# Kernel optimization log

Hardware: AMD Instinct MI355X
Metric: run time of the kernel (lower is better)

The kernel has to match this reference:

```python
import jax, jax.numpy as jnp
import numpy as np

BIAS = 1.0
SIGMA = 0.5
EPS = 1e-5


def _mrf_loss(gen, tar):
    # gen, tar: [N, C, H, W]
    N, C, H, W = tar.shape
    meanT = jnp.mean(tar, axis=1, keepdims=True)
    g = gen - meanT
    t = tar - meanT
    g = g / jnp.linalg.norm(g, ord=2, axis=1, keepdims=True)
    t = t / jnp.linalg.norm(t, ord=2, axis=1, keepdims=True)
    # 1x1-patch conv2d with target patches as filters == per-pixel cosine
    # correlation matrix: [N, P=H*W (target positions), H, W (gen positions)]
    tp = t.reshape(N, C, H * W)
    cd = jnp.einsum('nchw,ncp->nphw', g, tp)
    cd = -(cd - 1.0) / 2.0  # cosine distance in [0, 1]
    div = jnp.min(cd, axis=1, keepdims=True)
    rel = cd / (div + EPS)
    e = jnp.exp((BIAS - rel) / SIGMA)
    cs = e / jnp.sum(e, axis=1, keepdims=True)  # sum-normalize over P
    k_max_nc = jnp.max(cs.reshape(N, H * W, -1), axis=2)  # max over gen HW
    div_mrf = jnp.mean(k_max_nc, axis=1)
    return jnp.sum(-jnp.log(div_mrf))


def setup_inputs() -> dict:
    key = jax.random.key(0)
    k1, k2, k3, k4 = jax.random.split(key, 4)
    return {
        'gen3': jax.random.normal(k1, (4, 256, 56, 56), dtype=jnp.float32),
        'tar3': jax.random.normal(k2, (4, 256, 56, 56), dtype=jnp.float32),
        'gen4': jax.random.normal(k3, (4, 512, 28, 28), dtype=jnp.float32),
        'tar4': jax.random.normal(k4, (4, 512, 28, 28), dtype=jnp.float32),
    }


def reference(gen3, tar3, gen4, tar4):
    # weights = [0, 0, 0.5, 1, 0] over VGG relu1..relu5 features
    return 0.5 * _mrf_loss(gen3, tar3) + 1.0 * _mrf_loss(gen4, tar4)
```

## Files before the change

### kernel.cpp

```cpp
#include <hip/hip_runtime.h>
#include <math.h>

typedef __bf16 bf16x8 __attribute__((ext_vector_type(8)));
typedef float f32x4 __attribute__((ext_vector_type(4)));

#define EPSV 1e-5f
#define GLB(p) ((__attribute__((address_space(1))) void*)(p))
#define LDS(p) ((__attribute__((address_space(3))) void*)(p))

__device__ __forceinline__ unsigned fkey(float f) {
  unsigned b = __float_as_uint(f);
  return (b & 0x80000000u) ? ~b : (b | 0x80000000u);
}
__device__ __forceinline__ float funkey(unsigned k) {
  return __uint_as_float((k & 0x80000000u) ? (k & 0x7fffffffu) : ~k);
}

__global__ __launch_bounds__(256) void norm_kernel(
    const float* __restrict__ g3, const float* __restrict__ t3,
    __bf16* __restrict__ G3, __bf16* __restrict__ T3,
    const float* __restrict__ g4, const float* __restrict__ t4,
    __bf16* __restrict__ G4, __bf16* __restrict__ T4,
    float* __restrict__ ksum)
{
  if (blockIdx.z == 0 && blockIdx.y == 0 && threadIdx.x < 8)
    ksum[threadIdx.x] = 0.f;
  int lay = blockIdx.z >> 2, n = blockIdx.z & 3;
  const float *gen, *tar; __bf16 *Gh, *Th; int C, P, Ppad, PT, NWORK, NTOT, NG;
  if (lay == 0) { gen = g3; tar = t3; Gh = G3; Th = T3; C = 256; P = 3136; Ppad = 3200; PT = 32; NWORK = 98; NTOT = 100; NG = 8; }
  else          { gen = g4; tar = t4; Gh = G4; Th = T4; C = 512; P = 784;  Ppad = 896;  PT = 16; NWORK = 49; NTOT = 56;  NG = 16; }
  if (blockIdx.y >= (unsigned)NTOT) return;
  int pl, cg;
  if (lay == 0) { pl = threadIdx.x & 31; cg = threadIdx.x >> 5; }
  else          { pl = threadIdx.x & 15; cg = threadIdx.x >> 4; }
  int c0 = cg * 32;

  if (blockIdx.y >= (unsigned)NWORK) {
    int p = P + (blockIdx.y - NWORK) * PT + pl;
    if (p < Ppad) {
      __bf16* tp = Th + ((size_t)n * Ppad + p) * C + c0;
      __bf16* gp = Gh + ((size_t)n * Ppad + p) * C + c0;
      bf16x8 z;
      for (int j = 0; j < 8; j++) z[j] = (__bf16)0.f;
      for (int j = 0; j < 32; j += 8) { *(bf16x8*)(tp + j) = z; *(bf16x8*)(gp + j) = z; }
    }
    return;
  }

  int p = blockIdx.y * PT + pl;
  const float* tb = tar + (size_t)n * C * P + (size_t)c0 * P + p;
  const float* gb = gen + (size_t)n * C * P + (size_t)c0 * P + p;
  float tv[32], gv[32];
  float st = 0.f, sst = 0.f, sg = 0.f, ssg = 0.f;
#pragma unroll
  for (int j = 0; j < 32; j++) {
    tv[j] = tb[(size_t)j * P];
    gv[j] = gb[(size_t)j * P];
  }
#pragma unroll
  for (int j = 0; j < 32; j++) {
    st += tv[j]; sst += tv[j] * tv[j];
    sg += gv[j]; ssg += gv[j] * gv[j];
  }
  __shared__ f32x4 red[16][32];
  red[cg][pl] = f32x4{st, sst, sg, ssg};
  __syncthreads();
  for (int h = NG >> 1; h > 0; h >>= 1) {
    if (cg < h) {
      f32x4 a = red[cg][pl], b = red[cg + h][pl];
      red[cg][pl] = f32x4{a[0] + b[0], a[1] + b[1], a[2] + b[2], a[3] + b[3]};
    }
    __syncthreads();
  }
  f32x4 s = red[0][pl];
  float m = s[0] / (float)C;
  float vt = s[1] - s[0] * s[0] / (float)C;
  float vg = s[3] - 2.f * m * s[2] + (float)C * m * m;
  float it = rsqrtf(fmaxf(vt, 1e-30f));
  float ig = rsqrtf(fmaxf(vg, 1e-30f));
  __bf16* tp = Th + ((size_t)n * Ppad + p) * C + c0;
  __bf16* gp = Gh + ((size_t)n * Ppad + p) * C + c0;
#pragma unroll
  for (int j0 = 0; j0 < 32; j0 += 8) {
    bf16x8 to, go;
    for (int j = 0; j < 8; j++) {
      to[j] = (__bf16)((tv[j0 + j] - m) * it);
      go[j] = (__bf16)((gv[j0 + j] - m) * ig);
    }
    *(bf16x8*)(tp + j0) = to;
    *(bf16x8*)(gp + j0) = go;
  }
}

__global__ __launch_bounds__(256, 3) void gemm_kernel(
    const __bf16* __restrict__ A3, const __bf16* __restrict__ B3,
    __bf16* __restrict__ So3, unsigned* __restrict__ dk3,
    const __bf16* __restrict__ A4, const __bf16* __restrict__ B4,
    __bf16* __restrict__ So4, unsigned* __restrict__ dk4)
{
  __shared__ __attribute__((aligned(16))) char smem[37888];

  int id = blockIdx.x;
  const __bf16 *A, *B; __bf16* S; unsigned* dk;
  int C, Ppad, Qpad, Preal, NT, n, t;
  if (id < 2500) {
    n = id / 625; t = id - n * 625;
    A = A3; B = B3; S = So3; dk = dk3; C = 256; Ppad = 3200; Qpad = 3200; Preal = 3136; NT = 25;
  } else {
    id -= 2500;
    n = id / 49; t = id - n * 49;
    A = A4; B = B4; S = So4; dk = dk4; C = 512; Ppad = 896;  Qpad = 896;  Preal = 784;  NT = 7;
  }
  int bpb = NT * 8;
  int b = t / bpb, r = t - b * bpb;
  int rem = NT - b * 8;
  int h = rem < 8 ? rem : 8;
  int pt = b * 8 + r % h, qt = r / h;
  int p0 = pt * 128, q0 = qt * 128;

  int tid = threadIdx.x;
  int w = tid >> 6, lane = tid & 63;
  int lm = lane & 15, lq = lane >> 4;
  int wrow = (w >> 1) * 64, wcol = (w & 1) * 64;

  int srow = tid >> 2;
  int scol = ((tid & 3) ^ ((tid >> 3) & 3)) * 8;
  const __bf16* gA = A + ((size_t)n * Ppad + p0 + srow) * C + scol;
  const __bf16* gB = B + ((size_t)n * Qpad + q0 + srow) * C + scol;
  size_t rowoff = (size_t)64 * C;

  int sl = lq ^ ((lm >> 1) & 3);
  int aoff = (wrow + lm) * 64 + sl * 16;
  int boff = (wcol + lm) * 64 + sl * 16;

  f32x4 acc[4][4];
  for (int i = 0; i < 4; i++)
    for (int j = 0; j < 4; j++)
      acc[i][j] = f32x4{0.f, 0.f, 0.f, 0.f};

  for (int k0 = 0; k0 < C; k0 += 64) {
    __syncthreads();
#pragma unroll
    for (int sub = 0; sub < 2; sub++) {
      int kk = k0 + sub * 32;
      char* a = smem + sub * 8192 + w * 1024;
      char* bb = smem + 16384 + sub * 8192 + w * 1024;
      __builtin_amdgcn_global_load_lds(GLB(gA + kk), LDS(a), 16, 0, 0);
      __builtin_amdgcn_global_load_lds(GLB(gA + rowoff + kk), LDS(a + 4096), 16, 0, 0);
      __builtin_amdgcn_global_load_lds(GLB(gB + kk), LDS(bb), 16, 0, 0);
      __builtin_amdgcn_global_load_lds(GLB(gB + rowoff + kk), LDS(bb + 4096), 16, 0, 0);
    }
    __syncthreads();
#pragma unroll
    for (int sub = 0; sub < 2; sub++) {
      const char* ab = smem + sub * 8192;
      const char* bb = smem + 16384 + sub * 8192;
      bf16x8 af[4], bf[4];
      for (int i = 0; i < 4; i++) af[i] = *(const bf16x8*)(ab + aoff + i * 1024);
      for (int j = 0; j < 4; j++) bf[j] = *(const bf16x8*)(bb + boff + j * 1024);
      for (int i = 0; i < 4; i++)
        for (int j = 0; j < 4; j++)
          acc[i][j] = __builtin_amdgcn_mfma_f32_16x16x32_bf16(af[i], bf[j], acc[i][j], 0, 0, 0);
    }
  }

  float cm[4] = {-INFINITY, -INFINITY, -INFINITY, -INFINITY};
  for (int i = 0; i < 4; i++)
    for (int j = 0; j < 4; j++)
      for (int ri = 0; ri < 4; ri++) {
        int pr = p0 + wrow + i * 16 + lq * 4 + ri;
        if (pr < Preal) cm[j] = fmaxf(cm[j], (float)(__bf16)acc[i][j][ri]);
      }

  __syncthreads();
  for (int i = 0; i < 4; i++) {
    for (int j = 0; j < 4; j++) {
      int row = wrow + i * 16 + lq * 4;
      int col = wcol + j * 16 + lm;
      for (int ri = 0; ri < 4; ri++)
        *(__bf16*)(smem + (row + ri) * 296 + col * 2) = (__bf16)acc[i][j][ri];
    }
  }
  __syncthreads();
  __bf16* Sb = S + (size_t)n * Ppad * Qpad;
  int rr = tid >> 4, cc8 = (tid & 15) * 8;
  for (int r8 = 0; r8 < 8; r8++) {
    int row = r8 * 16 + rr;
    bf16x8 v = *(const bf16x8*)(smem + row * 296 + cc8 * 2);
    __builtin_nontemporal_store(v, (bf16x8*)(Sb + (size_t)(p0 + row) * Qpad + q0 + cc8));
  }

  for (int j = 0; j < 4; j++) {
    float v = cm[j];
    v = fmaxf(v, __shfl_xor(v, 16, 64));
    v = fmaxf(v, __shfl_xor(v, 32, 64));
    if (lq == 0 && v > -INFINITY) {
      int qc = q0 + wcol + j * 16 + lm;
      atomicMax(&dk[(size_t)n * Qpad + qc], fkey(v));
    }
  }
}

__global__ __launch_bounds__(256) void z_kernel(
    const __bf16* __restrict__ S3, const unsigned* __restrict__ dk3, float* __restrict__ Zp3,
    const __bf16* __restrict__ S4, const unsigned* __restrict__ dk4, float* __restrict__ Zp4)
{
  int id = blockIdx.x;
  const __bf16* S; const unsigned* dk; float* Zp;
  int Ppad, Qreal, Qpad, NSL, SLAB, n, qx, sy;
  if (id < 784) {
    n = id / 196; int r = id - n * 196; sy = r >> 1; qx = r & 1;
    S = S3; dk = dk3; Zp = Zp3; Ppad = 3200; Qreal = 3136; Qpad = 3200; NSL = 98; SLAB = 32;
  } else {
    id -= 784;
    n = id / 49; sy = id - n * 49; qx = 0;
    S = S4; dk = dk4; Zp = Zp4; Ppad = 896;  Qreal = 784;  Qpad = 896;  NSL = 49; SLAB = 16;
  }
  int q = (qx * 256 + threadIdx.x) * 8;
  if (q >= Qreal) return;
  float idv[8], nid[8];
  const unsigned* dkp = dk + (size_t)n * Qpad + q;
#pragma unroll
  for (int j = 0; j < 8; j++) {
    float mx = funkey(dkp[j]);
    float d = 0.5f * (1.f - mx) + EPSV;
    idv[j] = 1.f / d;
    nid[j] = -idv[j];
  }
  int p0 = sy * SLAB;
  const __bf16* Sp = S + (size_t)n * Ppad * Qpad + q;
  float acc[8] = {0.f, 0.f, 0.f, 0.f, 0.f, 0.f, 0.f, 0.f};
  for (int pb = 0; pb < SLAB; pb += 8) {
    bf16x8 sv[8];
#pragma unroll
    for (int r = 0; r < 8; r++)
      sv[r] = *(const bf16x8*)(Sp + (size_t)(p0 + pb + r) * Qpad);
#pragma unroll
    for (int r = 0; r < 8; r++)
      for (int j = 0; j < 8; j++)
        acc[j] += __expf(fmaf((float)sv[r][j], idv[j], nid[j]));
  }
  float* zp = Zp + ((size_t)n * NSL + sy) * Qpad + q;
  *(f32x4*)zp = f32x4{acc[0], acc[1], acc[2], acc[3]};
  *(f32x4*)(zp + 4) = f32x4{acc[4], acc[5], acc[6], acc[7]};
}

__global__ __launch_bounds__(256) void reduce_kernel(
    const float* __restrict__ Zp3, const unsigned* __restrict__ dk3,
    float* __restrict__ invd3, float* __restrict__ c3,
    const float* __restrict__ Zp4, const unsigned* __restrict__ dk4,
    float* __restrict__ invd4, float* __restrict__ c4)
{
  int lay = blockIdx.y >> 2, n = blockIdx.y & 3;
  const float* Zp; const unsigned* dk; float *invd, *c; int Qreal, Qpad, NSL;
  if (lay == 0) { Zp = Zp3; dk = dk3; invd = invd3; c = c3; Qreal = 3136; Qpad = 3200; NSL = 98; }
  else          { Zp = Zp4; dk = dk4; invd = invd4; c = c4; Qreal = 784;  Qpad = 896;  NSL = 49; }
  int q = blockIdx.x * 256 + threadIdx.x;
  if (q >= Qreal) return;
  float s0 = 0.f, s1 = 0.f, s2 = 0.f, s3 = 0.f;
  int sl = 0;
  for (; sl + 4 <= NSL; sl += 4) {
    s0 += Zp[((size_t)n * NSL + sl) * Qpad + q];
    s1 += Zp[((size_t)n * NSL + sl + 1) * Qpad + q];
    s2 += Zp[((size_t)n * NSL + sl + 2) * Qpad + q];
    s3 += Zp[((size_t)n * NSL + sl + 3) * Qpad + q];
  }
  for (; sl < NSL; sl++) s0 += Zp[((size_t)n * NSL + sl) * Qpad + q];
  float s = (s0 + s1) + (s2 + s3);
  float mx = funkey(dk[(size_t)n * Qpad + q]);
  float d = 0.5f * (1.f - mx) + EPSV;
  float idv = 1.f / d;
  invd[(size_t)n * Qpad + q] = idv;
  c[(size_t)n * Qpad + q] = -logf(s) - idv;
}

template<int ROWS>
__device__ __forceinline__ float rowmax_partial(
    const __bf16* __restrict__ Sp, const float* __restrict__ idp,
    const float* __restrict__ cp, int nq8, int Qpad)
{
  float m[ROWS];
#pragma unroll
  for (int r = 0; r < ROWS; r++) m[r] = -INFINITY;
  for (int i = threadIdx.x; i < nq8; i += 256) {
    f32x4 i0 = *(const f32x4*)(idp + (size_t)i * 8);
    f32x4 i1 = *(const f32x4*)(idp + (size_t)i * 8 + 4);
    f32x4 c0 = *(const f32x4*)(cp + (size_t)i * 8);
    f32x4 c1 = *(const f32x4*)(cp + (size_t)i * 8 + 4);
#pragma unroll
    for (int r = 0; r < ROWS; r++) {
      bf16x8 sv = *(const bf16x8*)(Sp + (size_t)r * Qpad + (size_t)i * 8);
#pragma unroll
      for (int j = 0; j < 4; j++)
        m[r] = fmaxf(m[r], fmaf((float)sv[j], i0[j], c0[j]));
#pragma unroll
      for (int j = 0; j < 4; j++)
        m[r] = fmaxf(m[r], fmaf((float)sv[j + 4], i1[j], c1[j]));
    }
  }
#pragma unroll
  for (int r = 0; r < ROWS; r++)
    for (int off = 32; off > 0; off >>= 1)
      m[r] = fmaxf(m[r], __shfl_xor(m[r], off, 64));
  __shared__ float red[4][ROWS];
  int w = threadIdx.x >> 6;
  if ((threadIdx.x & 63) == 0)
#pragma unroll
    for (int r = 0; r < ROWS; r++) red[w][r] = m[r];
  __syncthreads();
  float e = 0.f;
  if (threadIdx.x < ROWS) {
    int r = threadIdx.x;
    float mr = fmaxf(fmaxf(red[0][r], red[1][r]), fmaxf(red[2][r], red[3][r]));
    e = __expf(mr);
  }
  if (threadIdx.x < 64) {
#pragma unroll
    for (int off = 1; off < ROWS; off <<= 1)
      e += __shfl_xor(e, off, 64);
  }
  return e;
}

__global__ __launch_bounds__(256) void rowmax_kernel(
    const __bf16* __restrict__ S3, const float* __restrict__ invd3,
    const float* __restrict__ c3,
    const __bf16* __restrict__ S4, const float* __restrict__ invd4,
    const float* __restrict__ c4, float* __restrict__ ksum)
{
  int id = blockIdx.x;
  if (id < 392) {
    int n = id / 98, blk = id - n * 98;
    const __bf16* Sp = S3 + ((size_t)n * 3200 + blk * 32) * 3200;
    float e = rowmax_partial<32>(Sp, invd3 + (size_t)n * 3200,
                                 c3 + (size_t)n * 3200, 392, 3200);
    if (threadIdx.x == 0) atomicAdd(&ksum[n], e);
  } else {
    id -= 392;
    int n = id / 49, blk = id - n * 49;
    const __bf16* Sp = S4 + ((size_t)n * 896 + blk * 16) * 896;
    float e = rowmax_partial<16>(Sp, invd4 + (size_t)n * 896,
                                 c4 + (size_t)n * 896, 98, 896);
    if (threadIdx.x == 0) atomicAdd(&ksum[4 + n], e);
  }
}

__global__ void final_kernel(const float* __restrict__ ksum, float* __restrict__ out)
{
  if (threadIdx.x == 0) {
    float lp3 = logf(3136.f), lp4 = logf(784.f);
    float total = 0.f;
    for (int n = 0; n < 4; n++) total += 0.5f * (lp3 - logf(ksum[n]));
    for (int n = 0; n < 4; n++) total += 1.0f * (lp4 - logf(ksum[4 + n]));
    out[0] = total;
  }
}

extern "C" void kernel_launch(void* const* d_in, const int* in_sizes, int n_in,
                              void* d_out, int out_size, void* d_ws, size_t ws_size,
                              hipStream_t stream)
{
  const float* gen3 = (const float*)d_in[0];
  const float* tar3 = (const float*)d_in[1];
  const float* gen4 = (const float*)d_in[2];
  const float* tar4 = (const float*)d_in[3];

  char* ws = (char*)d_ws;
  size_t off = 0;
  auto take = [&](size_t bytes) { char* p = ws + off; off += bytes; return p; };

  unsigned* divkey3 = (unsigned*)take(51200);
  unsigned* divkey4 = (unsigned*)take(14336);
  size_t zero_bytes = off;
  __bf16* That3 = (__bf16*)take(6553600);
  __bf16* Ghat3 = (__bf16*)take(6553600);
  __bf16* That4 = (__bf16*)take(3670016);
  __bf16* Ghat4 = (__bf16*)take(3670016);
  __bf16* S3    = (__bf16*)take(81920000);
  __bf16* S4    = (__bf16*)take(6422528);
  float*  Zp3   = (float*) take(5017600);
  float*  Zp4   = (float*) take(702464);
  float* invd3  = (float*)take(51200);
  float* c3     = (float*)take(51200);
  float* ksum   = (float*)take(51200);
  float* invd4  = (float*)take(14336);
  float* c4     = (float*)take(14336);

  hipMemsetAsync(divkey3, 0, zero_bytes, stream);

  norm_kernel<<<dim3(1, 100, 8), 256, 0, stream>>>(gen3, tar3, Ghat3, That3,
                                                   gen4, tar4, Ghat4, That4, ksum);
  gemm_kernel<<<2696, 256, 0, stream>>>(That3, Ghat3, S3, divkey3,
                                        That4, Ghat4, S4, divkey4);
  z_kernel<<<980, 256, 0, stream>>>(S3, divkey3, Zp3,
                                    S4, divkey4, Zp4);
  reduce_kernel<<<dim3(13, 8), 256, 0, stream>>>(Zp3, divkey3, invd3, c3,
                                                 Zp4, divkey4, invd4, c4);
  rowmax_kernel<<<588, 256, 0, stream>>>(S3, invd3, c3,
                                         S4, invd4, c4, ksum);
  final_kernel<<<1, 64, 0, stream>>>(ksum, (float*)d_out);
}
```

Before: 195.3 us.

## Remap GEMM block ids across XCDs, use exp2 and atomic Z accumulation

```diff
diff --git a/kernel.cpp b/kernel.cpp
--- a/kernel.cpp
+++ b/kernel.cpp
@@ -100,7 +100,8 @@
 {
   __shared__ __attribute__((aligned(16))) char smem[37888];
 
-  int id = blockIdx.x;
+  int bid = blockIdx.x;
+  int id = (bid & 7) * 337 + (bid >> 3);
   const __bf16 *A, *B; __bf16* S; unsigned* dk;
   int C, Ppad, Qpad, Preal, NT, n, t;
   if (id < 2500) {
@@ -202,30 +203,31 @@
 }
 
 __global__ __launch_bounds__(256) void z_kernel(
-    const __bf16* __restrict__ S3, const unsigned* __restrict__ dk3, float* __restrict__ Zp3,
-    const __bf16* __restrict__ S4, const unsigned* __restrict__ dk4, float* __restrict__ Zp4)
+    const __bf16* __restrict__ S3, const unsigned* __restrict__ dk3, float* __restrict__ Z3,
+    const __bf16* __restrict__ S4, const unsigned* __restrict__ dk4, float* __restrict__ Z4)
 {
   int id = blockIdx.x;
-  const __bf16* S; const unsigned* dk; float* Zp;
-  int Ppad, Qreal, Qpad, NSL, SLAB, n, qx, sy;
+  const __bf16* S; const unsigned* dk; float* Z;
+  int Ppad, Qreal, Qpad, SLAB, n, qx, sy;
   if (id < 784) {
     n = id / 196; int r = id - n * 196; sy = r >> 1; qx = r & 1;
-    S = S3; dk = dk3; Zp = Zp3; Ppad = 3200; Qreal = 3136; Qpad = 3200; NSL = 98; SLAB = 32;
+    S = S3; dk = dk3; Z = Z3; Ppad = 3200; Qreal = 3136; Qpad = 3200; SLAB = 32;
   } else {
     id -= 784;
     n = id / 49; sy = id - n * 49; qx = 0;
-    S = S4; dk = dk4; Zp = Zp4; Ppad = 896;  Qreal = 784;  Qpad = 896;  NSL = 49; SLAB = 16;
+    S = S4; dk = dk4; Z = Z4; Ppad = 896;  Qreal = 784;  Qpad = 896;  SLAB = 16;
   }
   int q = (qx * 256 + threadIdx.x) * 8;
   if (q >= Qreal) return;
-  float idv[8], nid[8];
+  float idv2[8], nid2[8];
   const unsigned* dkp = dk + (size_t)n * Qpad + q;
 #pragma unroll
   for (int j = 0; j < 8; j++) {
     float mx = funkey(dkp[j]);
     float d = 0.5f * (1.f - mx) + EPSV;
-    idv[j] = 1.f / d;
-    nid[j] = -idv[j];
+    float iv = 1.4426950408889634f / d;
+    idv2[j] = iv;
+    nid2[j] = -iv;
   }
   int p0 = sy * SLAB;
   const __bf16* Sp = S + (size_t)n * Ppad * Qpad + q;
@@ -238,35 +240,26 @@
 #pragma unroll
     for (int r = 0; r < 8; r++)
       for (int j = 0; j < 8; j++)
-        acc[j] += __expf(fmaf((float)sv[r][j], idv[j], nid[j]));
-  }
-  float* zp = Zp + ((size_t)n * NSL + sy) * Qpad + q;
-  *(f32x4*)zp = f32x4{acc[0], acc[1], acc[2], acc[3]};
-  *(f32x4*)(zp + 4) = f32x4{acc[4], acc[5], acc[6], acc[7]};
+        acc[j] += exp2f(fmaf((float)sv[r][j], idv2[j], nid2[j]));
+  }
+  float* zp = Z + (size_t)n * Qpad + q;
+#pragma unroll
+  for (int j = 0; j < 8; j++) atomicAdd(zp + j, acc[j]);
 }
 
 __global__ __launch_bounds__(256) void reduce_kernel(
-    const float* __restrict__ Zp3, const unsigned* __restrict__ dk3,
+    const float* __restrict__ Z3, const unsigned* __restrict__ dk3,
     float* __restrict__ invd3, float* __restrict__ c3,
-    const float* __restrict__ Zp4, const unsigned* __restrict__ dk4,
+    const float* __restrict__ Z4, const unsigned* __restrict__ dk4,
     float* __restrict__ invd4, float* __restrict__ c4)
 {
   int lay = blockIdx.y >> 2, n = blockIdx.y & 3;
-  const float* Zp; const unsigned* dk; float *invd, *c; int Qreal, Qpad, NSL;
-  if (lay == 0) { Zp = Zp3; dk = dk3; invd = invd3; c = c3; Qreal = 3136; Qpad = 3200; NSL = 98; }
-  else          { Zp = Zp4; dk = dk4; invd = invd4; c = c4; Qreal = 784;  Qpad = 896;  NSL = 49; }
+  const float* Z; const unsigned* dk; float *invd, *c; int Qreal, Qpad;
+  if (lay == 0) { Z = Z3; dk = dk3; invd = invd3; c = c3; Qreal = 3136; Qpad = 3200; }
+  else          { Z = Z4; dk = dk4; invd = invd4; c = c4; Qreal = 784;  Qpad = 896;  }
   int q = blockIdx.x * 256 + threadIdx.x;
   if (q >= Qreal) return;
-  float s0 = 0.f, s1 = 0.f, s2 = 0.f, s3 = 0.f;
-  int sl = 0;
-  for (; sl + 4 <= NSL; sl += 4) {
-    s0 += Zp[((size_t)n * NSL + sl) * Qpad + q];
-    s1 += Zp[((size_t)n * NSL + sl + 1) * Qpad + q];
-    s2 += Zp[((size_t)n * NSL + sl + 2) * Qpad + q];
-    s3 += Zp[((size_t)n * NSL + sl + 3) * Qpad + q];
-  }
-  for (; sl < NSL; sl++) s0 += Zp[((size_t)n * NSL + sl) * Qpad + q];
-  float s = (s0 + s1) + (s2 + s3);
+  float s = Z[(size_t)n * Qpad + q];
   float mx = funkey(dk[(size_t)n * Qpad + q]);
   float d = 0.5f * (1.f - mx) + EPSV;
   float idv = 1.f / d;
@@ -371,6 +364,8 @@
 
   unsigned* divkey3 = (unsigned*)take(51200);
   unsigned* divkey4 = (unsigned*)take(14336);
+  float*    Z3      = (float*)   take(51200);
+  float*    Z4      = (float*)   take(14336);
   size_t zero_bytes = off;
   __bf16* That3 = (__bf16*)take(6553600);
   __bf16* Ghat3 = (__bf16*)take(6553600);
@@ -378,8 +373,6 @@
   __bf16* Ghat4 = (__bf16*)take(3670016);
   __bf16* S3    = (__bf16*)take(81920000);
   __bf16* S4    = (__bf16*)take(6422528);
-  float*  Zp3   = (float*) take(5017600);
-  float*  Zp4   = (float*) take(702464);
   float* invd3  = (float*)take(51200);
   float* c3     = (float*)take(51200);
   float* ksum   = (float*)take(51200);
@@ -392,10 +385,10 @@
                                                    gen4, tar4, Ghat4, That4, ksum);
   gemm_kernel<<<2696, 256, 0, stream>>>(That3, Ghat3, S3, divkey3,
                                         That4, Ghat4, S4, divkey4);
-  z_kernel<<<980, 256, 0, stream>>>(S3, divkey3, Zp3,
-                                    S4, divkey4, Zp4);
-  reduce_kernel<<<dim3(13, 8), 256, 0, stream>>>(Zp3, divkey3, invd3, c3,
-                                                 Zp4, divkey4, invd4, c4);
+  z_kernel<<<980, 256, 0, stream>>>(S3, divkey3, Z3,
+                                    S4, divkey4, Z4);
+  reduce_kernel<<<dim3(13, 8), 256, 0, stream>>>(Z3, divkey3, invd3, c3,
+                                                 Z4, divkey4, invd4, c4);
   rowmax_kernel<<<588, 256, 0, stream>>>(S3, invd3, c3,
                                          S4, invd4, c4, ksum);
   final_kernel<<<1, 64, 0, stream>>>(ksum, (float*)d_out);
```

Result: slower. 247.7 us (+26.8%).
